# Kernel tuning notes

Hardware: AMD Instinct MI355X
Metric: run time of the kernel (lower is better)

## Reference

```python
import jax, jax.numpy as jnp
import numpy as np

TEMPERATURE = 8.0


def setup_inputs() -> dict:
    key = jax.random.key(0)
    kq, kk, kv, km = jax.random.split(key, 4)
    B, H, S, D = 2, 16, 2048, 64
    q = jax.random.normal(kq, (B, H, S, D), dtype=jnp.float32)
    k = jax.random.normal(kk, (B, H, S, D), dtype=jnp.float32)
    v = jax.random.normal(kv, (B, H, S, D), dtype=jnp.float32)
    mask = jax.random.randint(km, (B, S, S), 0, 2, dtype=jnp.int32)
    return {"q": q, "k": k, "v": v, "mask": mask}


def reference(q, k, v, mask):
    # attn = q @ k^T / temperature  -> [B,H,Sq,Sk]
    attn = jnp.einsum("bhqd,bhkd->bhqk", q, k) / TEMPERATURE
    # mask: [B,Sq,Sk] -> [B,1,Sq,Sk]; masked where mask == 0
    m0 = (mask == 0)[:, None, :, :]
    attn = jnp.where(m0, -jnp.inf, attn)
    attn = jax.nn.softmax(attn, axis=-1)
    attn = jnp.where(m0, 0.0, attn)
    output = jnp.einsum("bhqk,bhkd->bhqd", attn, v)
    return (output, attn)
```

## Files before the change

kernel.cpp:

```cpp
#include <hip/hip_runtime.h>


#define S 2048
#define D 64
#define HH 16
#define BB 2
#define LDK 72

typedef __attribute__((ext_vector_type(8))) short short8;
typedef __attribute__((ext_vector_type(4))) float f32x4;
typedef __attribute__((ext_vector_type(2))) unsigned int u32x2;

__device__ __forceinline__ unsigned int packbf2(float a, float b) {
  union { __bf16 h[2]; unsigned int u; } r;
  r.h[0] = (__bf16)a;
  r.h[1] = (__bf16)b;
  return r.u;
}
__device__ __forceinline__ short8 cvt8(float4 a, float4 b) {
  union { unsigned int u[4]; short8 s; } r;
  r.u[0] = packbf2(a.x, a.y); r.u[1] = packbf2(a.z, a.w);
  r.u[2] = packbf2(b.x, b.y); r.u[3] = packbf2(b.z, b.w);
  return r.s;
}
__device__ __forceinline__ float4 qscale(float4 v) {
  return make_float4(v.x * 0.125f, v.y * 0.125f, v.z * 0.125f, v.w * 0.125f);
}

#define TRRD(dst, addr, off) \
  asm volatile("ds_read_b64_tr_b16 %0, %1 offset:" #off : "=v"(dst) : "v"(addr))

__global__ __launch_bounds__(256) void pack_mask_kernel(
    const int* __restrict__ m, unsigned long long* __restrict__ bits) {
  int wid = blockIdx.x * 4 + (threadIdx.x >> 6);
  int lane = threadIdx.x & 63;
  int v = m[(size_t)wid * 64 + lane];
  unsigned long long b = __ballot(v != 0);
  if (lane == 0) bits[wid] = b;
}

__global__ __launch_bounds__(256) void attn_kernel(
    const float* __restrict__ Qg, const float* __restrict__ Kg,
    const float* __restrict__ Vg, const unsigned long long* __restrict__ Mb,
    float* __restrict__ Og, float* __restrict__ Ag) {
  __shared__ alignas(128) unsigned short Vt[64 * 64];
  __shared__ unsigned short Kt[64 * LDK];

  const int tid = threadIdx.x;
  const int w = tid >> 6;
  const int lane = tid & 63;
  const int ln15 = lane & 15;
  const int quad = lane >> 4;

  const int bh = blockIdx.x;
  const int qtile = blockIdx.y;
  const int b = bh >> 4;
  const size_t qkvbase = (size_t)bh * S * D;
  const int q0 = qtile * 64;
  const int qrow = q0 + w * 16 + ln15;

  const float4* qp = reinterpret_cast<const float4*>(Qg + qkvbase + (size_t)qrow * D);
  short8 aq0, aq1;
  {
    float4 a0 = qscale(qp[quad * 2]), a1 = qscale(qp[quad * 2 + 1]);
    float4 b0 = qscale(qp[8 + quad * 2]), b1 = qscale(qp[8 + quad * 2 + 1]);
    aq0 = cvt8(a0, a1);
    aq1 = cvt8(b0, b1);
  }

  const unsigned long long* mrow = Mb + ((size_t)b * S + qrow) * (S / 64);

  const int trow = tid >> 2;
  const int tcol = (tid & 3) << 4;

  float lsum = 0.f;
  float4 kf0, kf1, kf2, kf3;
  {
    const float4* src = reinterpret_cast<const float4*>(Kg + qkvbase + (size_t)trow * D + tcol);
    kf0 = src[0]; kf1 = src[1]; kf2 = src[2]; kf3 = src[3];
  }
  unsigned long long mw = mrow[0];
  for (int t = 0; t < 32; ++t) {
    __syncthreads();
    *reinterpret_cast<short8*>(&Kt[trow * LDK + tcol]) = cvt8(kf0, kf1);
    *reinterpret_cast<short8*>(&Kt[trow * LDK + tcol + 8]) = cvt8(kf2, kf3);
    __syncthreads();
    if (t < 31) {
      const float4* src = reinterpret_cast<const float4*>(
          Kg + qkvbase + (size_t)((t + 1) * 64 + trow) * D + tcol);
      kf0 = src[0]; kf1 = src[1]; kf2 = src[2]; kf3 = src[3];
    }
    unsigned long long mwn = (t < 31) ? mrow[t + 1] : 0ULL;
#pragma unroll
    for (int kt = 0; kt < 4; ++kt) {
      short8 bk0 = *reinterpret_cast<const short8*>(&Kt[(kt * 16 + ln15) * LDK + (quad << 3)]);
      short8 bk1 = *reinterpret_cast<const short8*>(&Kt[(kt * 16 + ln15) * LDK + 32 + (quad << 3)]);
      f32x4 acc = {0.f, 0.f, 0.f, 0.f};
      acc = __builtin_amdgcn_mfma_f32_16x16x32_bf16(bk0, aq0, acc, 0, 0, 0);
      acc = __builtin_amdgcn_mfma_f32_16x16x32_bf16(bk1, aq1, acc, 0, 0, 0);
      unsigned int nib = (unsigned int)(mw >> (kt * 16 + quad * 4)) & 0xFu;
#pragma unroll
      for (int r = 0; r < 4; ++r) {
        float e = __expf(acc[r]);
        lsum += ((nib >> r) & 1u) ? e : 0.f;
      }
    }
    mw = mwn;
  }
  lsum += __shfl_xor(lsum, 16, 64);
  lsum += __shfl_xor(lsum, 32, 64);
  const float rinv = (lsum > 0.f) ? 1.f / lsum : 0.f;

  float* arow = Ag + ((size_t)bh * S + qrow) * S;
  f32x4 oacc[4] = {{0.f, 0.f, 0.f, 0.f}, {0.f, 0.f, 0.f, 0.f},
                   {0.f, 0.f, 0.f, 0.f}, {0.f, 0.f, 0.f, 0.f}};

  const unsigned int vbase = (unsigned int)(unsigned long long)(const void*)&Vt[0];
  const unsigned int vb = vbase + (unsigned int)(quad * 512 + ln15 * 8);
  const int vwoff = ((trow >> 2) * 4 + (tid & 3)) * 64 + (trow & 3) * 16;

  float4 vf0, vf1, vf2, vf3;
  {
    const float4* src = reinterpret_cast<const float4*>(Kg + qkvbase + (size_t)trow * D + tcol);
    kf0 = src[0]; kf1 = src[1]; kf2 = src[2]; kf3 = src[3];
    const float4* vs = reinterpret_cast<const float4*>(Vg + qkvbase + (size_t)trow * D + tcol);
    vf0 = vs[0]; vf1 = vs[1]; vf2 = vs[2]; vf3 = vs[3];
  }
  mw = mrow[0];
  for (int t = 0; t < 32; ++t) {
    __syncthreads();
    *reinterpret_cast<short8*>(&Kt[trow * LDK + tcol]) = cvt8(kf0, kf1);
    *reinterpret_cast<short8*>(&Kt[trow * LDK + tcol + 8]) = cvt8(kf2, kf3);
    *reinterpret_cast<short8*>(&Vt[vwoff]) = cvt8(vf0, vf1);
    *reinterpret_cast<short8*>(&Vt[vwoff + 8]) = cvt8(vf2, vf3);
    __syncthreads();
    if (t < 31) {
      const float4* src = reinterpret_cast<const float4*>(
          Kg + qkvbase + (size_t)((t + 1) * 64 + trow) * D + tcol);
      kf0 = src[0]; kf1 = src[1]; kf2 = src[2]; kf3 = src[3];
      const float4* vs = reinterpret_cast<const float4*>(
          Vg + qkvbase + (size_t)((t + 1) * 64 + trow) * D + tcol);
      vf0 = vs[0]; vf1 = vs[1]; vf2 = vs[2]; vf3 = vs[3];
    }
    unsigned long long mwn = (t < 31) ? mrow[t + 1] : 0ULL;
    const int k0 = t * 64;
    unsigned int apu[8];
#pragma unroll
    for (int kt = 0; kt < 4; ++kt) {
      short8 bk0 = *reinterpret_cast<const short8*>(&Kt[(kt * 16 + ln15) * LDK + (quad << 3)]);
      short8 bk1 = *reinterpret_cast<const short8*>(&Kt[(kt * 16 + ln15) * LDK + 32 + (quad << 3)]);
      f32x4 acc = {0.f, 0.f, 0.f, 0.f};
      acc = __builtin_amdgcn_mfma_f32_16x16x32_bf16(bk0, aq0, acc, 0, 0, 0);
      acc = __builtin_amdgcn_mfma_f32_16x16x32_bf16(bk1, aq1, acc, 0, 0, 0);
      unsigned int nib = (unsigned int)(mw >> (kt * 16 + quad * 4)) & 0xFu;
      f32x4 p;
#pragma unroll
      for (int r = 0; r < 4; ++r) {
        float e = __expf(acc[r]) * rinv;
        p[r] = ((nib >> r) & 1u) ? e : 0.f;
      }
      __builtin_nontemporal_store(p, reinterpret_cast<f32x4*>(arow + k0 + kt * 16 + quad * 4));
      apu[kt * 2] = packbf2(p[0], p[1]);
      apu[kt * 2 + 1] = packbf2(p[2], p[3]);
    }
    u32x2 x0, x1, x2, x3, x4, x5, x6, x7, x8, x9, x10, x11, x12, x13, x14, x15;
    TRRD(x0, vb, 0);     TRRD(x1, vb, 2048);
    TRRD(x2, vb, 128);   TRRD(x3, vb, 2176);
    TRRD(x4, vb, 256);   TRRD(x5, vb, 2304);
    TRRD(x6, vb, 384);   TRRD(x7, vb, 2432);
    TRRD(x8, vb, 4096);  TRRD(x9, vb, 6144);
    TRRD(x10, vb, 4224); TRRD(x11, vb, 6272);
    TRRD(x12, vb, 4352); TRRD(x13, vb, 6400);
    TRRD(x14, vb, 4480); TRRD(x15, vb, 6528);
    asm volatile("s_waitcnt lgkmcnt(0)" ::: "memory");
    __builtin_amdgcn_sched_barrier(0);
    union Frag { unsigned int u[4]; u32x2 d[2]; short8 s; };
    Frag ap0, ap1, bv;
    ap0.u[0] = apu[0]; ap0.u[1] = apu[1]; ap0.u[2] = apu[2]; ap0.u[3] = apu[3];
    ap1.u[0] = apu[4]; ap1.u[1] = apu[5]; ap1.u[2] = apu[6]; ap1.u[3] = apu[7];
    bv.d[0] = x0;  bv.d[1] = x1;
    oacc[0] = __builtin_amdgcn_mfma_f32_16x16x32_bf16(ap0.s, bv.s, oacc[0], 0, 0, 0);
    bv.d[0] = x2;  bv.d[1] = x3;
    oacc[1] = __builtin_amdgcn_mfma_f32_16x16x32_bf16(ap0.s, bv.s, oacc[1], 0, 0, 0);
    bv.d[0] = x4;  bv.d[1] = x5;
    oacc[2] = __builtin_amdgcn_mfma_f32_16x16x32_bf16(ap0.s, bv.s, oacc[2], 0, 0, 0);
    bv.d[0] = x6;  bv.d[1] = x7;
    oacc[3] = __builtin_amdgcn_mfma_f32_16x16x32_bf16(ap0.s, bv.s, oacc[3], 0, 0, 0);
    bv.d[0] = x8;  bv.d[1] = x9;
    oacc[0] = __builtin_amdgcn_mfma_f32_16x16x32_bf16(ap1.s, bv.s, oacc[0], 0, 0, 0);
    bv.d[0] = x10; bv.d[1] = x11;
    oacc[1] = __builtin_amdgcn_mfma_f32_16x16x32_bf16(ap1.s, bv.s, oacc[1], 0, 0, 0);
    bv.d[0] = x12; bv.d[1] = x13;
    oacc[2] = __builtin_amdgcn_mfma_f32_16x16x32_bf16(ap1.s, bv.s, oacc[2], 0, 0, 0);
    bv.d[0] = x14; bv.d[1] = x15;
    oacc[3] = __builtin_amdgcn_mfma_f32_16x16x32_bf16(ap1.s, bv.s, oacc[3], 0, 0, 0);
    mw = mwn;
  }

#pragma unroll
  for (int c = 0; c < 4; ++c) {
#pragma unroll
    for (int r = 0; r < 4; ++r) {
      Og[qkvbase + (size_t)(q0 + w * 16 + quad * 4 + r) * D + c * 16 + ln15] = oacc[c][r];
    }
  }
}

extern "C" void kernel_launch(void* const* d_in, const int* in_sizes, int n_in,
                              void* d_out, int out_size, void* d_ws, size_t ws_size,
                              hipStream_t stream) {
  const float* q = (const float*)d_in[0];
  const float* k = (const float*)d_in[1];
  const float* v = (const float*)d_in[2];
  const int* m = (const int*)d_in[3];
  float* outp = (float*)d_out;
  float* attnp = outp + (size_t)BB * HH * S * D;
  unsigned long long* bits = (unsigned long long*)d_ws;

  const int nwords = BB * S * (S / 64);
  pack_mask_kernel<<<nwords / 4, 256, 0, stream>>>(m, bits);
  dim3 grid(BB * HH, S / 64);
  attn_kernel<<<grid, 256, 0, stream>>>(q, k, v, bits, outp, attnp);
}
```

Measured before the change: 795.5 us.

## Pre-convert K/V to bf16, read K directly from global, double-buffer V

```diff
diff --git a/kernel.cpp b/kernel.cpp
--- a/kernel.cpp
+++ b/kernel.cpp
@@ -5,7 +5,7 @@
 #define D 64
 #define HH 16
 #define BB 2
-#define LDK 72
+#define NE (BB * HH * S * D)
 
 typedef __attribute__((ext_vector_type(8))) short short8;
 typedef __attribute__((ext_vector_type(4))) float f32x4;
@@ -23,8 +23,14 @@
   r.u[2] = packbf2(b.x, b.y); r.u[3] = packbf2(b.z, b.w);
   return r.s;
 }
+#define QSC 0.1803368801111204f
 __device__ __forceinline__ float4 qscale(float4 v) {
-  return make_float4(v.x * 0.125f, v.y * 0.125f, v.z * 0.125f, v.w * 0.125f);
+  return make_float4(v.x * QSC, v.y * QSC, v.z * QSC, v.w * QSC);
+}
+__device__ __forceinline__ float exp2fast(float x) {
+  float r;
+  asm("v_exp_f32 %0, %1" : "=v"(r) : "v"(x));
+  return r;
 }
 
 #define TRRD(dst, addr, off) \
@@ -39,12 +45,25 @@
   if (lane == 0) bits[wid] = b;
 }
 
+__global__ __launch_bounds__(256) void cvt_kv_kernel(
+    const float* __restrict__ K, const float* __restrict__ V,
+    unsigned short* __restrict__ Kb, unsigned short* __restrict__ Vb) {
+  size_t i = ((size_t)blockIdx.x * 256 + threadIdx.x) * 8;
+  const float* s;
+  unsigned short* d;
+  if (i < (size_t)NE) { s = K + i; d = Kb + i; }
+  else { s = V + (i - NE); d = Vb + (i - NE); }
+  float4 a = *reinterpret_cast<const float4*>(s);
+  float4 b = *reinterpret_cast<const float4*>(s + 4);
+  *reinterpret_cast<short8*>(d) = cvt8(a, b);
+}
+
+template <int PRE>
 __global__ __launch_bounds__(256) void attn_kernel(
-    const float* __restrict__ Qg, const float* __restrict__ Kg,
-    const float* __restrict__ Vg, const unsigned long long* __restrict__ Mb,
+    const float* __restrict__ Qg, const void* __restrict__ Kx,
+    const void* __restrict__ Vx, const unsigned long long* __restrict__ Mb,
     float* __restrict__ Og, float* __restrict__ Ag) {
-  __shared__ alignas(128) unsigned short Vt[64 * 64];
-  __shared__ unsigned short Kt[64 * LDK];
+  __shared__ alignas(128) unsigned short Vt[2][4096];
 
   const int tid = threadIdx.x;
   const int w = tid >> 6;
@@ -70,42 +89,45 @@
 
   const unsigned long long* mrow = Mb + ((size_t)b * S + qrow) * (S / 64);
 
-  const int trow = tid >> 2;
-  const int tcol = (tid & 3) << 4;
+  const unsigned short* pkh =
+      reinterpret_cast<const unsigned short*>(Kx) + qkvbase + (size_t)ln15 * D + quad * 8;
+  const float* pkf =
+      reinterpret_cast<const float*>(Kx) + qkvbase + (size_t)ln15 * D + quad * 8;
+
+  auto loadK = [&](int row, short8& b0, short8& b1) {
+    if constexpr (PRE) {
+      const unsigned short* p = pkh + (size_t)row * D;
+      b0 = *reinterpret_cast<const short8*>(p);
+      b1 = *reinterpret_cast<const short8*>(p + 32);
+    } else {
+      const float* p = pkf + (size_t)row * D;
+      float4 a0 = *reinterpret_cast<const float4*>(p);
+      float4 a1 = *reinterpret_cast<const float4*>(p + 4);
+      float4 c0 = *reinterpret_cast<const float4*>(p + 32);
+      float4 c1 = *reinterpret_cast<const float4*>(p + 36);
+      b0 = cvt8(a0, a1);
+      b1 = cvt8(c0, c1);
+    }
+  };
 
   float lsum = 0.f;
-  float4 kf0, kf1, kf2, kf3;
-  {
-    const float4* src = reinterpret_cast<const float4*>(Kg + qkvbase + (size_t)trow * D + tcol);
-    kf0 = src[0]; kf1 = src[1]; kf2 = src[2]; kf3 = src[3];
-  }
-  unsigned long long mw = mrow[0];
+#pragma unroll 2
   for (int t = 0; t < 32; ++t) {
-    __syncthreads();
-    *reinterpret_cast<short8*>(&Kt[trow * LDK + tcol]) = cvt8(kf0, kf1);
-    *reinterpret_cast<short8*>(&Kt[trow * LDK + tcol + 8]) = cvt8(kf2, kf3);
-    __syncthreads();
-    if (t < 31) {
-      const float4* src = reinterpret_cast<const float4*>(
-          Kg + qkvbase + (size_t)((t + 1) * 64 + trow) * D + tcol);
-      kf0 = src[0]; kf1 = src[1]; kf2 = src[2]; kf3 = src[3];
-    }
-    unsigned long long mwn = (t < 31) ? mrow[t + 1] : 0ULL;
+    unsigned long long mw = mrow[t];
 #pragma unroll
     for (int kt = 0; kt < 4; ++kt) {
-      short8 bk0 = *reinterpret_cast<const short8*>(&Kt[(kt * 16 + ln15) * LDK + (quad << 3)]);
-      short8 bk1 = *reinterpret_cast<const short8*>(&Kt[(kt * 16 + ln15) * LDK + 32 + (quad << 3)]);
+      short8 bk0, bk1;
+      loadK(t * 64 + kt * 16, bk0, bk1);
       f32x4 acc = {0.f, 0.f, 0.f, 0.f};
       acc = __builtin_amdgcn_mfma_f32_16x16x32_bf16(bk0, aq0, acc, 0, 0, 0);
       acc = __builtin_amdgcn_mfma_f32_16x16x32_bf16(bk1, aq1, acc, 0, 0, 0);
       unsigned int nib = (unsigned int)(mw >> (kt * 16 + quad * 4)) & 0xFu;
 #pragma unroll
       for (int r = 0; r < 4; ++r) {
-        float e = __expf(acc[r]);
+        float e = exp2fast(acc[r]);
         lsum += ((nib >> r) & 1u) ? e : 0.f;
       }
     }
-    mw = mwn;
   }
   lsum += __shfl_xor(lsum, 16, 64);
   lsum += __shfl_xor(lsum, 32, 64);
@@ -115,40 +137,60 @@
   f32x4 oacc[4] = {{0.f, 0.f, 0.f, 0.f}, {0.f, 0.f, 0.f, 0.f},
                    {0.f, 0.f, 0.f, 0.f}, {0.f, 0.f, 0.f, 0.f}};
 
-  const unsigned int vbase = (unsigned int)(unsigned long long)(const void*)&Vt[0];
-  const unsigned int vb = vbase + (unsigned int)(quad * 512 + ln15 * 8);
+  const int trow = tid >> 2;
+  const int d0c = (tid & 3) << 4;
   const int vwoff = ((trow >> 2) * 4 + (tid & 3)) * 64 + (trow & 3) * 16;
-
-  float4 vf0, vf1, vf2, vf3;
-  {
-    const float4* src = reinterpret_cast<const float4*>(Kg + qkvbase + (size_t)trow * D + tcol);
-    kf0 = src[0]; kf1 = src[1]; kf2 = src[2]; kf3 = src[3];
-    const float4* vs = reinterpret_cast<const float4*>(Vg + qkvbase + (size_t)trow * D + tcol);
-    vf0 = vs[0]; vf1 = vs[1]; vf2 = vs[2]; vf3 = vs[3];
-  }
-  mw = mrow[0];
+  const unsigned int vb0 =
+      (unsigned int)(unsigned long long)(const void*)&Vt[0][0] +
+      (unsigned int)(quad * 512 + ln15 * 8);
+
+  const unsigned short* pvh =
+      reinterpret_cast<const unsigned short*>(Vx) + qkvbase + (size_t)trow * D + d0c;
+  const float* pvf =
+      reinterpret_cast<const float*>(Vx) + qkvbase + (size_t)trow * D + d0c;
+
+  short8 hv0, hv1;
+  float4 fv0, fv1, fv2, fv3;
+  auto loadV = [&](int t) {
+    if constexpr (PRE) {
+      const unsigned short* p = pvh + (size_t)t * 64 * D;
+      hv0 = *reinterpret_cast<const short8*>(p);
+      hv1 = *reinterpret_cast<const short8*>(p + 8);
+    } else {
+      const float* p = pvf + (size_t)t * 64 * D;
+      fv0 = reinterpret_cast<const float4*>(p)[0];
+      fv1 = reinterpret_cast<const float4*>(p)[1];
+      fv2 = reinterpret_cast<const float4*>(p)[2];
+      fv3 = reinterpret_cast<const float4*>(p)[3];
+    }
+  };
+  auto writeV = [&](int buf) {
+    unsigned short* dst = &Vt[buf][vwoff];
+    if constexpr (PRE) {
+      *reinterpret_cast<short8*>(dst) = hv0;
+      *reinterpret_cast<short8*>(dst + 8) = hv1;
+    } else {
+      *reinterpret_cast<short8*>(dst) = cvt8(fv0, fv1);
+      *reinterpret_cast<short8*>(dst + 8) = cvt8(fv2, fv3);
+    }
+  };
+
+  loadV(0);
+  writeV(0);
+  loadV(1);
+  __syncthreads();
+
   for (int t = 0; t < 32; ++t) {
-    __syncthreads();
-    *reinterpret_cast<short8*>(&Kt[trow * LDK + tcol]) = cvt8(kf0, kf1);
-    *reinterpret_cast<short8*>(&Kt[trow * LDK + tcol + 8]) = cvt8(kf2, kf3);
-    *reinterpret_cast<short8*>(&Vt[vwoff]) = cvt8(vf0, vf1);
-    *reinterpret_cast<short8*>(&Vt[vwoff + 8]) = cvt8(vf2, vf3);
-    __syncthreads();
-    if (t < 31) {
-      const float4* src = reinterpret_cast<const float4*>(
-          Kg + qkvbase + (size_t)((t + 1) * 64 + trow) * D + tcol);
-      kf0 = src[0]; kf1 = src[1]; kf2 = src[2]; kf3 = src[3];
-      const float4* vs = reinterpret_cast<const float4*>(
-          Vg + qkvbase + (size_t)((t + 1) * 64 + trow) * D + tcol);
-      vf0 = vs[0]; vf1 = vs[1]; vf2 = vs[2]; vf3 = vs[3];
-    }
-    unsigned long long mwn = (t < 31) ? mrow[t + 1] : 0ULL;
+    const int cur = t & 1;
+    if (t < 31) writeV(cur ^ 1);
+    if (t < 30) loadV(t + 2);
+    unsigned long long mw = mrow[t];
     const int k0 = t * 64;
     unsigned int apu[8];
 #pragma unroll
     for (int kt = 0; kt < 4; ++kt) {
-      short8 bk0 = *reinterpret_cast<const short8*>(&Kt[(kt * 16 + ln15) * LDK + (quad << 3)]);
-      short8 bk1 = *reinterpret_cast<const short8*>(&Kt[(kt * 16 + ln15) * LDK + 32 + (quad << 3)]);
+      short8 bk0, bk1;
+      loadK(t * 64 + kt * 16, bk0, bk1);
       f32x4 acc = {0.f, 0.f, 0.f, 0.f};
       acc = __builtin_amdgcn_mfma_f32_16x16x32_bf16(bk0, aq0, acc, 0, 0, 0);
       acc = __builtin_amdgcn_mfma_f32_16x16x32_bf16(bk1, aq1, acc, 0, 0, 0);
@@ -156,13 +198,14 @@
       f32x4 p;
 #pragma unroll
       for (int r = 0; r < 4; ++r) {
-        float e = __expf(acc[r]) * rinv;
+        float e = exp2fast(acc[r]) * rinv;
         p[r] = ((nib >> r) & 1u) ? e : 0.f;
       }
       __builtin_nontemporal_store(p, reinterpret_cast<f32x4*>(arow + k0 + kt * 16 + quad * 4));
       apu[kt * 2] = packbf2(p[0], p[1]);
       apu[kt * 2 + 1] = packbf2(p[2], p[3]);
     }
+    const unsigned int vb = vb0 + (unsigned int)(cur << 13);
     u32x2 x0, x1, x2, x3, x4, x5, x6, x7, x8, x9, x10, x11, x12, x13, x14, x15;
     TRRD(x0, vb, 0);     TRRD(x1, vb, 2048);
     TRRD(x2, vb, 128);   TRRD(x3, vb, 2176);
@@ -194,7 +237,7 @@
     oacc[2] = __builtin_amdgcn_mfma_f32_16x16x32_bf16(ap1.s, bv.s, oacc[2], 0, 0, 0);
     bv.d[0] = x14; bv.d[1] = x15;
     oacc[3] = __builtin_amdgcn_mfma_f32_16x16x32_bf16(ap1.s, bv.s, oacc[3], 0, 0, 0);
-    mw = mwn;
+    __syncthreads();
   }
 
 #pragma unroll
@@ -215,10 +258,20 @@
   const int* m = (const int*)d_in[3];
   float* outp = (float*)d_out;
   float* attnp = outp + (size_t)BB * HH * S * D;
+
+  const size_t bitsBytes = (size_t)BB * S * (S / 64) * 8;
   unsigned long long* bits = (unsigned long long*)d_ws;
+  unsigned short* Kb = (unsigned short*)((char*)d_ws + bitsBytes);
+  unsigned short* Vb = Kb + (size_t)NE;
+  const bool pre = ws_size >= bitsBytes + 2 * (size_t)NE * sizeof(unsigned short);
 
   const int nwords = BB * S * (S / 64);
   pack_mask_kernel<<<nwords / 4, 256, 0, stream>>>(m, bits);
   dim3 grid(BB * HH, S / 64);
-  attn_kernel<<<grid, 256, 0, stream>>>(q, k, v, bits, outp, attnp);
-}
+  if (pre) {
+    cvt_kv_kernel<<<(2 * (size_t)NE / 8) / 256, 256, 0, stream>>>(k, v, Kb, Vb);
+    attn_kernel<1><<<grid, 256, 0, stream>>>(q, Kb, Vb, bits, outp, attnp);
+  } else {
+    attn_kernel<0><<<grid, 256, 0, stream>>>(q, k, v, bits, outp, attnp);
+  }
+}
```

Result: slower. 846.4 us (+6.4%).
